# Optimization experiments

Hardware: AMD Instinct MI355X
Metric: run time of the kernel (lower is better)

## Reference

```python
import jax, jax.numpy as jnp
import numpy as np

B, NPER, F, D, E, NUM_STEPS = 256, 512, 256, 32, 524288, 4
N = B * NPER
INIT_TAU, TAU_SCALE, STEP_ALPHA = 0.1, 0.5, 5.0


def setup_inputs() -> dict:
    key = jax.random.key(0)
    ks = jax.random.split(key, 10)
    x_start = jax.random.uniform(ks[0], (N,), jnp.float32, 0.1, 1.0)   # strictly positive iterate
    x_solution = jax.random.uniform(ks[1], (N,), jnp.float32, 0.0, 1.0)
    q = jax.random.normal(ks[2], (N,), jnp.float32)
    edge_src = jax.random.randint(ks[3], (E,), 0, N, jnp.int32)
    edge_dst = jax.random.randint(ks[4], (E,), 0, N, jnp.int32)
    vals_batch = jnp.repeat(jnp.arange(B, dtype=jnp.int32), NPER)      # equal-sized graphs
    proj_matrix = jax.random.normal(ks[5], (B, NPER, F), jnp.float32) / np.float32(np.sqrt(NPER))
    W_in = jax.random.normal(ks[6], (2, D), jnp.float32) / np.float32(np.sqrt(2.0))
    b_in = jnp.zeros((D,), jnp.float32)
    W_msg = jax.random.normal(ks[7], (D, D), jnp.float32) / np.float32(np.sqrt(D))
    b_msg = jnp.zeros((D,), jnp.float32)
    W_out = jax.random.normal(ks[8], (D, 1), jnp.float32) / np.float32(np.sqrt(D))
    b_out = jnp.zeros((1,), jnp.float32)
    return {"x_start": x_start, "x_solution": x_solution, "q": q,
            "proj_matrix": proj_matrix, "W_in": W_in, "b_in": b_in,
            "W_msg": W_msg, "b_msg": b_msg, "W_out": W_out, "b_out": b_out,
            "edge_src": edge_src, "edge_dst": edge_dst, "vals_batch": vals_batch}


def _l1_normalize(x, batch):
    # per-graph L1 normalization: x / sum_i |x_i| over the graph segment
    s = jax.ops.segment_sum(jnp.abs(x), batch, num_segments=B)
    return x / (s[batch] + 1e-12)


def _line_search(x, d, batch, max_alpha):
    # largest per-graph alpha s.t. x + alpha*d >= 0, capped at max_alpha
    ratio = jnp.where(d < 0, x / jnp.maximum(-d, 1e-12), max_alpha)
    a = jnp.clip(jax.ops.segment_min(ratio, batch, num_segments=B), 0.0, max_alpha)
    return a[batch]  # gathered back to per-node


def _gnn(xs, q, edge_src, edge_dst, W_in, b_in, W_msg, b_msg, W_out, b_out):
    h = jax.nn.relu(jnp.stack([xs, q], axis=-1) @ W_in + b_in)      # [N, D]
    m = h[edge_src] @ W_msg + b_msg                                  # [E, D]
    agg = jax.ops.segment_sum(m, edge_dst, num_segments=N)          # [N, D]
    h2 = jax.nn.relu(h + agg)
    return h2 @ W_out[:, 0] + b_out[0]                               # [N]


def reference(x_start, x_solution, q, proj_matrix, W_in, b_in, W_msg, b_msg,
              W_out, b_out, edge_src, edge_dst, vals_batch):
    tau = INIT_TAU
    xs = x_start
    preds, labels = [], []
    for _ in range(NUM_STEPS):
        pred = _gnn(xs, q, edge_src, edge_dst, W_in, b_in, W_msg, b_msg, W_out, b_out)
        preds.append(pred)
        labels.append(_l1_normalize(x_solution - xs, vals_batch))
        p = _l1_normalize(jax.lax.stop_gradient(pred), vals_batch)   # .detach() in torch
        direction = p + 3.0 * tau / (xs + tau)
        tau = max(tau * TAU_SCALE, 1e-5)
        # to_dense_batch with equal graph sizes == reshape; project onto nullspace basis
        dd = direction.reshape(B, NPER)
        df = jnp.einsum('bnf,bn->bf', proj_matrix, dd)               # [B, F]
        pproj = jnp.einsum('bnf,bf->bn', proj_matrix, df).reshape(-1)  # [N]
        alpha = _line_search(xs, pproj, vals_batch, STEP_ALPHA) * 0.995
        xs = xs + alpha * pproj
    return jnp.stack(preds, axis=1), jnp.stack(labels, axis=1)       # each [N, NUM_STEPS]
```

## Files before the change

### kernel.cpp

```cpp
#include <hip/hip_runtime.h>

#define BB 256
#define NPER 512
#define FF 256
#define DD 32
#define EE 524288
#define NN (BB*NPER)
#define NSTEPS 4

__device__ __forceinline__ float bflo(unsigned u) { return __uint_as_float(u << 16); }
__device__ __forceinline__ float bfhi(unsigned u) { return __uint_as_float(u & 0xFFFF0000u); }
__device__ __forceinline__ unsigned rtn_bf16(unsigned u) {
    return (u + 0x7FFFu + ((u >> 16) & 1u)) >> 16;
}


__global__ void k_degpack(const int* __restrict__ dst, unsigned* __restrict__ deg,
                          const float* __restrict__ xs0, const float* __restrict__ q,
                          float2* __restrict__ xq) {
    int t = blockIdx.x * blockDim.x + threadIdx.x;
    if (t < NN) { float2 v; v.x = xs0[t]; v.y = q[t]; xq[t] = v; }
    atomicAdd(&deg[dst[t]], 1u);
}

__global__ __launch_bounds__(256) void k_alloc(const unsigned* __restrict__ deg,
                                               unsigned* __restrict__ gcur,
                                               unsigned* __restrict__ rowstart,
                                               unsigned* __restrict__ cursor) {
    __shared__ unsigned r[256];
    __shared__ unsigned base;
    int t = threadIdx.x;
    int i = blockIdx.x * 256 + t;
    unsigned d = deg[i];
    r[t] = d;
    __syncthreads();
    for (int o = 1; o < 256; o <<= 1) {
        unsigned v = (t >= o) ? r[t - o] : 0u;
        __syncthreads();
        r[t] += v;
        __syncthreads();
    }
    if (t == 255) base = atomicAdd(gcur, r[255]);
    __syncthreads();
    unsigned excl = r[t] - d + base;
    rowstart[i] = excl;
    cursor[i] = excl;
}

__global__ void k_fill(const int* __restrict__ src, const int* __restrict__ dst,
                       unsigned* __restrict__ cursor, int* __restrict__ csr_src) {
    int e = blockIdx.x * blockDim.x + threadIdx.x;
    unsigned pos = atomicAdd(&cursor[dst[e]], 1u);
    csr_src[pos] = src[e];
}

template<int MODE>
__global__ __launch_bounds__(1024) void k_mega(const float* __restrict__ Pf,
                                               unsigned short* __restrict__ Pbf,
                                               const float2* __restrict__ xq_cur,
                                               float2* __restrict__ xq_nxt,
                                               const float* __restrict__ xsol,
                                               const float* __restrict__ Win,
                                               const float* __restrict__ bin,
                                               const float* __restrict__ Wmsg,
                                               const float* __restrict__ bmsg,
                                               const float* __restrict__ Wout,
                                               const float* __restrict__ bout,
                                               const unsigned* __restrict__ rowstart,
                                               const unsigned* __restrict__ deg,
                                               const int* __restrict__ csr_src,
                                               float* __restrict__ out_preds,
                                               float* __restrict__ out_labels,
                                               float tau, int step) {
    __shared__ float pred_l[NPER];
    __shared__ float dd_l[NPER], x_l[NPER], pp_l[NPER];
    __shared__ float sl[16 * FF];
    __shared__ float dfl[FF];
    __shared__ float redA[16], redB[16];
    int b = blockIdx.x;
    int t = threadIdx.x;
    int w = t >> 6, lane = t & 63;
    int gbase = b * NPER;

    {
        int d = lane & 31;
        int half = lane >> 5;
        float w0 = Win[d], w1 = Win[DD + d], b0 = bin[d];
        float wcol[DD];
        #pragma unroll
        for (int k = 0; k < DD; ++k) wcol[k] = Wmsg[k * DD + d];
        float wo = Wout[d];
        for (int pass = 0; pass < 16; ++pass) {
            int node = pass * 32 + w * 2 + half;
            int i = gbase + node;
            unsigned rs = rowstart[i];
            unsigned dg = deg[i];
            unsigned nfull = dg < 32u ? dg : 32u;
            float xv = 0.f, qv = 0.f;
            if ((unsigned)d < nfull) {
                int sv = csr_src[rs + d];
                float2 v = xq_cur[sv];
                xv = v.x; qv = v.y;
            }
            float s = 0.f;
            for (unsigned j = 0; j < nfull; ++j) {
                float xj = __shfl(xv, (int)j, 32);
                float qj = __shfl(qv, (int)j, 32);
                s += fmaxf(xj * w0 + qj * w1 + b0, 0.f);
            }
            for (unsigned j = 32; j < dg; ++j) {
                int sv = csr_src[rs + j];
                float2 v = xq_cur[sv];
                s += fmaxf(v.x * w0 + v.y * w1 + b0, 0.f);
            }
            float2 self = xq_cur[i];
            float hval = fmaxf(self.x * w0 + self.y * w1 + b0, 0.f);
            float agg = (float)dg * bmsg[d];
            #pragma unroll
            for (int k = 0; k < DD; ++k) agg += __shfl(s, k, 32) * wcol[k];
            float h2 = fmaxf(hval + agg, 0.f);
            float v = h2 * wo;
            #pragma unroll
            for (int o = 16; o > 0; o >>= 1) v += __shfl_down(v, o, 32);
            if (d == 0) {
                float pr = v + bout[0];
                pred_l[node] = pr;
                out_preds[(size_t)i * NSTEPS + step] = pr;
            }
        }
    }
    __syncthreads();

    float x = 0.f, r = 0.f, p = 0.f, a1 = 0.f, a2 = 0.f;
    if (t < NPER) {
        x = xq_cur[gbase + t].x;
        r = xsol[gbase + t] - x;
        p = pred_l[t];
        a1 = fabsf(r); a2 = fabsf(p);
    }
    #pragma unroll
    for (int o = 32; o > 0; o >>= 1) {
        a1 += __shfl_down(a1, o, 64);
        a2 += __shfl_down(a2, o, 64);
    }
    if (lane == 0) { redA[w] = a1; redB[w] = a2; }
    __syncthreads();
    float Sr = 1e-12f, Sp = 1e-12f;
    #pragma unroll
    for (int k = 0; k < 16; ++k) { Sr += redA[k]; Sp += redB[k]; }
    if (t < NPER) out_labels[(size_t)(gbase + t) * NSTEPS + step] = r / Sr;
    if (MODE == 2) return;
    if (t < NPER) {
        x_l[t] = x;
        dd_l[t] = p / Sp + 3.0f * tau / (x + tau);
    }
    __syncthreads();

    size_t pbase = ((size_t)(gbase + w * 32)) * FF + 4 * lane;
    float4 acc = {0.f, 0.f, 0.f, 0.f};
    if (MODE == 0) {
        const float4* Pr = (const float4*)(Pf + pbase);
        uint2* Pw = (uint2*)(Pbf + pbase);
        #pragma unroll
        for (int nb = 0; nb < 4; ++nb) {
            float4 pv[8];
            #pragma unroll
            for (int k = 0; k < 8; ++k) pv[k] = Pr[(size_t)(nb * 8 + k) * 64];
            #pragma unroll
            for (int k = 0; k < 8; ++k) {
                int n = nb * 8 + k;
                float sc = dd_l[w * 32 + n];
                acc.x += pv[k].x * sc; acc.y += pv[k].y * sc;
                acc.z += pv[k].z * sc; acc.w += pv[k].w * sc;
                unsigned u0 = rtn_bf16(__float_as_uint(pv[k].x));
                unsigned u1 = rtn_bf16(__float_as_uint(pv[k].y));
                unsigned u2 = rtn_bf16(__float_as_uint(pv[k].z));
                unsigned u3 = rtn_bf16(__float_as_uint(pv[k].w));
                uint2 o2; o2.x = u0 | (u1 << 16); o2.y = u2 | (u3 << 16);
                Pw[(size_t)n * 64] = o2;
            }
        }
    } else {
        const uint2* Pr = (const uint2*)(Pbf + pbase);
        #pragma unroll
        for (int nb = 0; nb < 4; ++nb) {
            uint2 pv[8];
            #pragma unroll
            for (int k = 0; k < 8; ++k) pv[k] = Pr[(size_t)(nb * 8 + k) * 64];
            #pragma unroll
            for (int k = 0; k < 8; ++k) {
                float sc = dd_l[w * 32 + nb * 8 + k];
                acc.x += bflo(pv[k].x) * sc; acc.y += bfhi(pv[k].x) * sc;
                acc.z += bflo(pv[k].y) * sc; acc.w += bfhi(pv[k].y) * sc;
            }
        }
    }
    ((float4*)sl)[w * 64 + lane] = acc;
    __syncthreads();
    if (t < FF) {
        float v = 0.f;
        #pragma unroll
        for (int k = 0; k < 16; ++k) v += sl[k * FF + t];
        dfl[t] = v;
    }
    __syncthreads();

    {
        int g = t >> 5, l5 = t & 31;
        float4 dfa = ((const float4*)dfl)[l5 * 2];
        float4 dfb4 = ((const float4*)dfl)[l5 * 2 + 1];
        const uint4* Pr4 = (const uint4*)(Pbf + (size_t)(gbase + g * 16) * FF) + l5;
        #pragma unroll
        for (int nb = 0; nb < 4; ++nb) {
            uint4 pv[4];
            #pragma unroll
            for (int k = 0; k < 4; ++k) pv[k] = Pr4[(size_t)(nb * 4 + k) * 32];
            #pragma unroll
            for (int k = 0; k < 4; ++k) {
                float a = bflo(pv[k].x) * dfa.x + bfhi(pv[k].x) * dfa.y
                        + bflo(pv[k].y) * dfa.z + bfhi(pv[k].y) * dfa.w
                        + bflo(pv[k].z) * dfb4.x + bfhi(pv[k].z) * dfb4.y
                        + bflo(pv[k].w) * dfb4.z + bfhi(pv[k].w) * dfb4.w;
                #pragma unroll
                for (int o = 16; o > 0; o >>= 1) a += __shfl_down(a, o, 32);
                if (l5 == 0) pp_l[g * 16 + nb * 4 + k] = a;
            }
        }
    }
    __syncthreads();

    float d = 0.f, m = 5.0f;
    if (t < NPER) {
        d = pp_l[t];
        m = (d < 0.f) ? (x_l[t] / fmaxf(-d, 1e-12f)) : 5.0f;
    }
    #pragma unroll
    for (int o = 32; o > 0; o >>= 1) m = fminf(m, __shfl_down(m, o, 64));
    if (lane == 0) redA[w] = m;
    __syncthreads();
    float mm = redA[0];
    #pragma unroll
    for (int k = 1; k < 16; ++k) mm = fminf(mm, redA[k]);
    float alpha = fminf(fmaxf(mm, 0.f), 5.0f) * 0.995f;
    if (t < NPER) {
        float2 o2;
        o2.x = x_l[t] + alpha * d;
        o2.y = xq_cur[gbase + t].y;
        xq_nxt[gbase + t] = o2;
    }
}


extern "C" void kernel_launch(void* const* d_in, const int* in_sizes, int n_in,
                              void* d_out, int out_size, void* d_ws, size_t ws_size,
                              hipStream_t stream) {
    const float* x_start = (const float*)d_in[0];
    const float* x_sol   = (const float*)d_in[1];
    const float* q       = (const float*)d_in[2];
    const float* P       = (const float*)d_in[3];
    const float* Win     = (const float*)d_in[4];
    const float* bin     = (const float*)d_in[5];
    const float* Wmsg    = (const float*)d_in[6];
    const float* bmsg    = (const float*)d_in[7];
    const float* Wout    = (const float*)d_in[8];
    const float* bout    = (const float*)d_in[9];
    const int*   esrc    = (const int*)d_in[10];
    const int*   edst    = (const int*)d_in[11];

    float* out_preds  = (float*)d_out;
    float* out_labels = (float*)d_out + (size_t)NN * NSTEPS;

    float* w = (float*)d_ws;
    unsigned* deg  = (unsigned*)w; w += NN;
    unsigned* gcur = (unsigned*)w; w += 2;
    float2* xqA = (float2*)w; w += 2 * (size_t)NN;
    float2* xqB = (float2*)w; w += 2 * (size_t)NN;
    unsigned* rowstart = (unsigned*)w; w += NN;
    unsigned* cursor   = (unsigned*)w; w += NN;
    int* csr_src       = (int*)w;      w += EE;
    unsigned short* Pbf = (unsigned short*)w;

    hipMemsetAsync(deg, 0, (NN + 2) * sizeof(unsigned), stream);
    k_degpack<<<EE / 256, 256, 0, stream>>>(edst, deg, x_start, q, xqA);
    k_alloc<<<NN / 256, 256, 0, stream>>>(deg, gcur, rowstart, cursor);
    k_fill<<<EE / 256, 256, 0, stream>>>(esrc, edst, cursor, csr_src);

    k_mega<0><<<BB, 1024, 0, stream>>>(P, Pbf, xqA, xqB, x_sol, Win, bin, Wmsg, bmsg,
                                       Wout, bout, rowstart, deg, csr_src,
                                       out_preds, out_labels, 0.1f, 0);
    k_mega<1><<<BB, 1024, 0, stream>>>(P, Pbf, xqB, xqA, x_sol, Win, bin, Wmsg, bmsg,
                                       Wout, bout, rowstart, deg, csr_src,
                                       out_preds, out_labels, 0.05f, 1);
    k_mega<1><<<BB, 1024, 0, stream>>>(P, Pbf, xqA, xqB, x_sol, Win, bin, Wmsg, bmsg,
                                       Wout, bout, rowstart, deg, csr_src,
                                       out_preds, out_labels, 0.025f, 2);
    k_mega<2><<<BB, 1024, 0, stream>>>(P, Pbf, xqB, (float2*)nullptr, x_sol, Win, bin,
                                       Wmsg, bmsg, Wout, bout, rowstart, deg, csr_src,
                                       out_preds, out_labels, 0.0125f, 3);
}
```

Baseline: 493.9 us.

## Keep projection tile in registers for back-projection instead of reloading from global

Each thread keeps the bf16-packed slice of the projection matrix it loaded for the forward projection in 64 registers, then reuses it for the back-projection. This replaces the second global read of the bf16 matrix with a 64-lane xor-shuffle reduction per node row, and folds the line-search ratio and min into that same loop, which drops one barrier. The costs are much higher register pressure (launch bounds now set to one block) and a full-wave reduction per row in place of half-wave reductions.

```diff
diff --git a/kernel.cpp b/kernel.cpp
--- a/kernel.cpp
+++ b/kernel.cpp
@@ -55,23 +55,23 @@
 }
 
 template<int MODE>
-__global__ __launch_bounds__(1024) void k_mega(const float* __restrict__ Pf,
-                                               unsigned short* __restrict__ Pbf,
-                                               const float2* __restrict__ xq_cur,
-                                               float2* __restrict__ xq_nxt,
-                                               const float* __restrict__ xsol,
-                                               const float* __restrict__ Win,
-                                               const float* __restrict__ bin,
-                                               const float* __restrict__ Wmsg,
-                                               const float* __restrict__ bmsg,
-                                               const float* __restrict__ Wout,
-                                               const float* __restrict__ bout,
-                                               const unsigned* __restrict__ rowstart,
-                                               const unsigned* __restrict__ deg,
-                                               const int* __restrict__ csr_src,
-                                               float* __restrict__ out_preds,
-                                               float* __restrict__ out_labels,
-                                               float tau, int step) {
+__global__ __launch_bounds__(1024, 1) void k_mega(const float* __restrict__ Pf,
+                                                  unsigned short* __restrict__ Pbf,
+                                                  const float2* __restrict__ xq_cur,
+                                                  float2* __restrict__ xq_nxt,
+                                                  const float* __restrict__ xsol,
+                                                  const float* __restrict__ Win,
+                                                  const float* __restrict__ bin,
+                                                  const float* __restrict__ Wmsg,
+                                                  const float* __restrict__ bmsg,
+                                                  const float* __restrict__ Wout,
+                                                  const float* __restrict__ bout,
+                                                  const unsigned* __restrict__ rowstart,
+                                                  const unsigned* __restrict__ deg,
+                                                  const int* __restrict__ csr_src,
+                                                  float* __restrict__ out_preds,
+                                                  float* __restrict__ out_labels,
+                                                  float tau, int step) {
     __shared__ float pred_l[NPER];
     __shared__ float dd_l[NPER], x_l[NPER], pp_l[NPER];
     __shared__ float sl[16 * FF];
@@ -157,45 +157,52 @@
     __syncthreads();
 
     size_t pbase = ((size_t)(gbase + w * 32)) * FF + 4 * lane;
-    float4 acc = {0.f, 0.f, 0.f, 0.f};
-    if (MODE == 0) {
-        const float4* Pr = (const float4*)(Pf + pbase);
-        uint2* Pw = (uint2*)(Pbf + pbase);
-        #pragma unroll
-        for (int nb = 0; nb < 4; ++nb) {
-            float4 pv[8];
-            #pragma unroll
-            for (int k = 0; k < 8; ++k) pv[k] = Pr[(size_t)(nb * 8 + k) * 64];
-            #pragma unroll
-            for (int k = 0; k < 8; ++k) {
-                int n = nb * 8 + k;
-                float sc = dd_l[w * 32 + n];
-                acc.x += pv[k].x * sc; acc.y += pv[k].y * sc;
-                acc.z += pv[k].z * sc; acc.w += pv[k].w * sc;
-                unsigned u0 = rtn_bf16(__float_as_uint(pv[k].x));
-                unsigned u1 = rtn_bf16(__float_as_uint(pv[k].y));
-                unsigned u2 = rtn_bf16(__float_as_uint(pv[k].z));
-                unsigned u3 = rtn_bf16(__float_as_uint(pv[k].w));
-                uint2 o2; o2.x = u0 | (u1 << 16); o2.y = u2 | (u3 << 16);
-                Pw[(size_t)n * 64] = o2;
+    unsigned pl[64];
+    {
+        float4 acc = {0.f, 0.f, 0.f, 0.f};
+        if (MODE == 0) {
+            const float4* Pr = (const float4*)(Pf + pbase);
+            uint2* Pw = (uint2*)(Pbf + pbase);
+            #pragma unroll
+            for (int nb = 0; nb < 8; ++nb) {
+                float4 pv[4];
+                #pragma unroll
+                for (int k = 0; k < 4; ++k) pv[k] = Pr[(size_t)(nb * 4 + k) * 64];
+                #pragma unroll
+                for (int k = 0; k < 4; ++k) {
+                    int n = nb * 4 + k;
+                    float sc = dd_l[w * 32 + n];
+                    acc.x += pv[k].x * sc; acc.y += pv[k].y * sc;
+                    acc.z += pv[k].z * sc; acc.w += pv[k].w * sc;
+                    unsigned u0 = rtn_bf16(__float_as_uint(pv[k].x));
+                    unsigned u1 = rtn_bf16(__float_as_uint(pv[k].y));
+                    unsigned u2 = rtn_bf16(__float_as_uint(pv[k].z));
+                    unsigned u3 = rtn_bf16(__float_as_uint(pv[k].w));
+                    unsigned lo = u0 | (u1 << 16), hi = u2 | (u3 << 16);
+                    uint2 o2; o2.x = lo; o2.y = hi;
+                    Pw[(size_t)n * 64] = o2;
+                    pl[2 * n] = lo; pl[2 * n + 1] = hi;
+                }
+            }
+        } else {
+            const uint2* Pr = (const uint2*)(Pbf + pbase);
+            #pragma unroll
+            for (int nb = 0; nb < 4; ++nb) {
+                uint2 pv[8];
+                #pragma unroll
+                for (int k = 0; k < 8; ++k) pv[k] = Pr[(size_t)(nb * 8 + k) * 64];
+                #pragma unroll
+                for (int k = 0; k < 8; ++k) {
+                    int n = nb * 8 + k;
+                    float sc = dd_l[w * 32 + n];
+                    acc.x += bflo(pv[k].x) * sc; acc.y += bfhi(pv[k].x) * sc;
+                    acc.z += bflo(pv[k].y) * sc; acc.w += bfhi(pv[k].y) * sc;
+                    pl[2 * n] = pv[k].x; pl[2 * n + 1] = pv[k].y;
+                }
             }
         }
-    } else {
-        const uint2* Pr = (const uint2*)(Pbf + pbase);
-        #pragma unroll
-        for (int nb = 0; nb < 4; ++nb) {
-            uint2 pv[8];
-            #pragma unroll
-            for (int k = 0; k < 8; ++k) pv[k] = Pr[(size_t)(nb * 8 + k) * 64];
-            #pragma unroll
-            for (int k = 0; k < 8; ++k) {
-                float sc = dd_l[w * 32 + nb * 8 + k];
-                acc.x += bflo(pv[k].x) * sc; acc.y += bfhi(pv[k].x) * sc;
-                acc.z += bflo(pv[k].y) * sc; acc.w += bfhi(pv[k].y) * sc;
-            }
-        }
-    }
-    ((float4*)sl)[w * 64 + lane] = acc;
+        ((float4*)sl)[w * 64 + lane] = acc;
+    }
     __syncthreads();
     if (t < FF) {
         float v = 0.f;
@@ -205,46 +212,29 @@
     }
     __syncthreads();
 
-    {
-        int g = t >> 5, l5 = t & 31;
-        float4 dfa = ((const float4*)dfl)[l5 * 2];
-        float4 dfb4 = ((const float4*)dfl)[l5 * 2 + 1];
-        const uint4* Pr4 = (const uint4*)(Pbf + (size_t)(gbase + g * 16) * FF) + l5;
+    float4 dfv = ((const float4*)dfl)[lane];
+    float mloc = 5.0f;
+    #pragma unroll
+    for (int n = 0; n < 32; ++n) {
+        float pr = bflo(pl[2 * n]) * dfv.x + bfhi(pl[2 * n]) * dfv.y
+                 + bflo(pl[2 * n + 1]) * dfv.z + bfhi(pl[2 * n + 1]) * dfv.w;
         #pragma unroll
-        for (int nb = 0; nb < 4; ++nb) {
-            uint4 pv[4];
-            #pragma unroll
-            for (int k = 0; k < 4; ++k) pv[k] = Pr4[(size_t)(nb * 4 + k) * 32];
-            #pragma unroll
-            for (int k = 0; k < 4; ++k) {
-                float a = bflo(pv[k].x) * dfa.x + bfhi(pv[k].x) * dfa.y
-                        + bflo(pv[k].y) * dfa.z + bfhi(pv[k].y) * dfa.w
-                        + bflo(pv[k].z) * dfb4.x + bfhi(pv[k].z) * dfb4.y
-                        + bflo(pv[k].w) * dfb4.z + bfhi(pv[k].w) * dfb4.w;
-                #pragma unroll
-                for (int o = 16; o > 0; o >>= 1) a += __shfl_down(a, o, 32);
-                if (l5 == 0) pp_l[g * 16 + nb * 4 + k] = a;
-            }
-        }
-    }
-    __syncthreads();
-
-    float d = 0.f, m = 5.0f;
-    if (t < NPER) {
-        d = pp_l[t];
-        m = (d < 0.f) ? (x_l[t] / fmaxf(-d, 1e-12f)) : 5.0f;
-    }
-    #pragma unroll
-    for (int o = 32; o > 0; o >>= 1) m = fminf(m, __shfl_down(m, o, 64));
-    if (lane == 0) redA[w] = m;
-    __syncthreads();
+        for (int o = 1; o < 64; o <<= 1) pr += __shfl_xor(pr, o, 64);
+        if (lane == 0) pp_l[w * 32 + n] = pr;
+        float xr = x_l[w * 32 + n];
+        float ratio = (pr < 0.f) ? (xr / fmaxf(-pr, 1e-12f)) : 5.0f;
+        mloc = fminf(mloc, ratio);
+    }
+    if (lane == 0) redA[w] = mloc;
+    __syncthreads();
+
     float mm = redA[0];
     #pragma unroll
     for (int k = 1; k < 16; ++k) mm = fminf(mm, redA[k]);
     float alpha = fminf(fmaxf(mm, 0.f), 5.0f) * 0.995f;
     if (t < NPER) {
         float2 o2;
-        o2.x = x_l[t] + alpha * d;
+        o2.x = x_l[t] + alpha * pp_l[t];
         o2.y = xq_cur[gbase + t].y;
         xq_nxt[gbase + t] = o2;
     }
```

Result: slower. 545.8 us (+10.5%).
